# Kernel optimization log

Hardware: AMD Instinct MI355X
Metric: run time of the kernel (lower is better)

Reference implementation:

```python
import jax, jax.numpy as jnp
import numpy as np

B, T, C = 2, 2048, 1024
H, D = 16, 64


def setup_inputs() -> dict:
    key = jax.random.key(0)
    ks = jax.random.split(key, 5)
    s = 1.0 / np.sqrt(C)  # keep projections well-scaled
    return {
        "x": jax.random.normal(ks[0], (B, T, C), dtype=jnp.float32),
        "wq": jax.random.normal(ks[1], (C, C), dtype=jnp.float32) * s,
        "wk": jax.random.normal(ks[2], (C, C), dtype=jnp.float32) * s,
        "wv": jax.random.normal(ks[3], (C, C), dtype=jnp.float32) * s,
        "wo": jax.random.normal(ks[4], (C, C), dtype=jnp.float32) * s,
    }


def reference(x, wq, wk, wv, wo):
    # nn.Linear(d,d,bias=False): y = x @ W.T ; weights stored [out,in]
    q = (x @ wq.T).reshape(B, T, H, D).transpose(0, 2, 1, 3)  # [B,H,T,D]
    k = (x @ wk.T).reshape(B, T, H, D).transpose(0, 2, 1, 3)
    v = (x @ wv.T).reshape(B, T, H, D).transpose(0, 2, 1, 3)
    scale = jnp.sqrt(jnp.float32(D))
    scores = jnp.einsum("bhtd,bhsd->bhts", q, k) / scale  # [B,H,T,T]
    # additive causal mask: -inf above the diagonal
    causal = jnp.tril(jnp.ones((T, T), dtype=bool))
    scores = jnp.where(causal[None, None], scores, jnp.float32(-1e9))
    weights = jax.nn.softmax(scores, axis=-1)
    out = jnp.einsum("bhts,bhsd->bhtd", weights, v)  # [B,H,T,D]
    out = out.transpose(0, 2, 1, 3).reshape(B, T, C)
    return out @ wo.T
```

## Files before the change

### kernel.cpp

```cpp
#include <hip/hip_runtime.h>
#include <stdint.h>

#define B_ 2
#define T_ 2048
#define C_ 1024
#define H_ 16
#define D_ 64
#define M_ (B_*T_)

typedef __attribute__((ext_vector_type(8))) short bf16x8;
typedef __attribute__((ext_vector_type(4))) short bf16x4;
typedef __attribute__((ext_vector_type(4))) float f32x4;
typedef unsigned short u16;

#define MFMA32(a, b, c) __builtin_amdgcn_mfma_f32_16x16x32_bf16((a), (b), (c), 0, 0, 0)

__device__ __forceinline__ u16 f2bf(float f) {
  union { float f; uint32_t u; } v; v.f = f;
  uint32_t u = v.u;
  return (u16)((u + 0x7fffu + ((u >> 16) & 1u)) >> 16);
}

__device__ __forceinline__ float exp2_fast(float x) { return __builtin_amdgcn_exp2f(x); }

typedef const __attribute__((address_space(1))) void* gas_t;
typedef __attribute__((address_space(3))) void* las_t;
__device__ __forceinline__ void gld_lds16(const void* g, void* l) {
  __builtin_amdgcn_global_load_lds((gas_t)g, (las_t)l, 16, 0, 0);
}

__global__ void cvt_bf16(const float* __restrict__ src, u16* __restrict__ dst) {
  int i = (blockIdx.x * blockDim.x + threadIdx.x) * 4;
  float4 v = *(const float4*)(src + i);
  ushort4 o;
  o.x = f2bf(v.x); o.y = f2bf(v.y); o.z = f2bf(v.z); o.w = f2bf(v.w);
  *(ushort4*)(dst + i) = o;
}

__global__ void cvt_bf16_w4(const float* __restrict__ s0, const float* __restrict__ s1,
                            const float* __restrict__ s2, const float* __restrict__ s3,
                            u16* __restrict__ d0, u16* __restrict__ d1,
                            u16* __restrict__ d2, u16* __restrict__ d3) {
  const float* s; u16* d;
  switch (blockIdx.y) {
    case 0: s = s0; d = d0; break;
    case 1: s = s1; d = d1; break;
    case 2: s = s2; d = d2; break;
    default: s = s3; d = d3; break;
  }
  int i = (blockIdx.x * blockDim.x + threadIdx.x) * 4;
  float4 v = *(const float4*)(s + i);
  ushort4 o;
  o.x = f2bf(v.x); o.y = f2bf(v.y); o.z = f2bf(v.z); o.w = f2bf(v.w);
  *(ushort4*)(d + i) = o;
}

__device__ __forceinline__ void gemm_core(const u16* __restrict__ A,
                                          const u16* __restrict__ W,
                                          int m0, int n0, int Kt,
                                          f32x4 acc[4][4])
{
  __shared__ u16 As[128*64];
  __shared__ u16 Bs[128*64];
  const int t = threadIdx.x;
  const int lane = t & 63;
  const int wave = t >> 6;
  const int q = lane >> 4;
  const int l15 = lane & 15;
  const int wm = (wave >> 1) * 64;
  const int wn = (wave & 1) * 64;

  #pragma unroll
  for (int i = 0; i < 4; ++i)
    #pragma unroll
    for (int j = 0; j < 4; ++j)
      acc[i][j] = (f32x4){0.f, 0.f, 0.f, 0.f};

  for (int k0 = 0; k0 < Kt; k0 += 64) {
    #pragma unroll
    for (int r = 0; r < 4; ++r) {
      int Lc = r * 256 + t;
      int row = Lc >> 3;
      int gcc = (Lc & 7) ^ (row & 7);
      gld_lds16(A + (size_t)(m0 + row) * Kt + k0 + gcc * 8, As + Lc * 8);
    }
    #pragma unroll
    for (int r = 0; r < 4; ++r) {
      int Lc = r * 256 + t;
      int row = Lc >> 3;
      int gcc = (Lc & 7) ^ (row & 7);
      gld_lds16(W + (size_t)(n0 + row) * Kt + k0 + gcc * 8, Bs + Lc * 8);
    }
    __syncthreads();

    #pragma unroll
    for (int kk = 0; kk < 2; ++kk) {
      bf16x8 af[4], bfr[4];
      #pragma unroll
      for (int i = 0; i < 4; ++i) {
        int m = wm + i * 16 + l15;
        int ch = (kk * 4 + q) ^ (m & 7);
        af[i] = *(const bf16x8*)(As + m * 64 + ch * 8);
      }
      #pragma unroll
      for (int j = 0; j < 4; ++j) {
        int n = wn + j * 16 + l15;
        int ch = (kk * 4 + q) ^ (n & 7);
        bfr[j] = *(const bf16x8*)(Bs + n * 64 + ch * 8);
      }
      #pragma unroll
      for (int i = 0; i < 4; ++i)
        #pragma unroll
        for (int j = 0; j < 4; ++j)
          acc[i][j] = MFMA32(af[i], bfr[j], acc[i][j]);
    }
    __syncthreads();
  }
}

#define QSCALE 0.1803368801111244f
__global__ __launch_bounds__(256, 3)
void gemm_qkv(const u16* __restrict__ X,
              const u16* __restrict__ Wq, const u16* __restrict__ Wk,
              const u16* __restrict__ Wv,
              u16* __restrict__ Q, u16* __restrict__ K, u16* __restrict__ Vt)
{
  const int bm = blockIdx.x;
  const int bn = blockIdx.y;
  const int seg = bn >> 3;
  const int n0 = (bn & 7) * 128;
  const u16* W = (seg == 0) ? Wq : ((seg == 1) ? Wk : Wv);

  f32x4 acc[4][4];
  gemm_core(X, W, bm * 128, n0, C_, acc);

  const int t = threadIdx.x, lane = t & 63, wave = t >> 6;
  const int q = lane >> 4, l15 = lane & 15;
  const int wm = (wave >> 1) * 64, wn = (wave & 1) * 64;
  const float scale = (seg == 0) ? QSCALE : 1.0f;

  #pragma unroll
  for (int i = 0; i < 4; ++i) {
    #pragma unroll
    for (int j = 0; j < 4; ++j) {
      const int mbase = bm * 128 + wm + i * 16 + q * 4;
      const int n = n0 + wn + j * 16 + l15;
      const int h = n >> 6, d = n & 63;
      if (seg < 2) {
        u16* dst = (seg == 0) ? Q : K;
        #pragma unroll
        for (int r = 0; r < 4; ++r) {
          const int m = mbase + r;
          const int b = m >> 11, tt = m & (T_ - 1);
          size_t idx = (((size_t)(b * H_ + h)) * T_ + tt) * D_ + d;
          dst[idx] = f2bf(acc[i][j][r] * scale);
        }
      } else {
        const int b = mbase >> 11, tt = mbase & (T_ - 1);
        const int ttp = (tt & ~31) | ((tt & 12) << 1) | ((tt & 16) >> 2);
        size_t idx = (((size_t)(b * H_ + h)) * D_ + d) * T_ + ttp;
        ushort4 pk;
        pk.x = f2bf(acc[i][j][0]); pk.y = f2bf(acc[i][j][1]);
        pk.z = f2bf(acc[i][j][2]); pk.w = f2bf(acc[i][j][3]);
        *(ushort4*)(Vt + idx) = pk;
      }
    }
  }
}

__global__ __launch_bounds__(256, 2)
void attn(const u16* __restrict__ Q, const u16* __restrict__ K,
          const u16* __restrict__ Vt, u16* __restrict__ Att)
{
  __shared__ u16 Ks[2][64 * 64];
  __shared__ u16 Vs[2][64 * 64];
  const int t = threadIdx.x;
  const int lane = t & 63, wave = t >> 6;
  const int q = lane >> 4, l15 = lane & 15;
  const int pr = blockIdx.x;
  const int bh = blockIdx.y;
  const int qbA = pr * 64;
  const int qbB = (31 - pr) * 64;
  const u16* Qp = Q + (size_t)bh * T_ * D_;
  const u16* Kp = K + (size_t)bh * T_ * D_;
  const u16* Vp = Vt + (size_t)bh * D_ * T_;

  const int rowA = qbA + 4 * l15 + wave;
  const int rowB = qbB + 4 * l15 + wave;
  const u16* qra = Qp + (size_t)rowA * 64;
  const u16* qrb = Qp + (size_t)rowB * 64;
  const bf16x8 aqA0 = *(const bf16x8*)(qra + q * 8);
  const bf16x8 aqA1 = *(const bf16x8*)(qra + 32 + q * 8);
  const bf16x8 aqB0 = *(const bf16x8*)(qrb + q * 8);
  const bf16x8 aqB1 = *(const bf16x8*)(qrb + 32 + q * 8);

  f32x4 oA[4], oB[4];
  #pragma unroll
  for (int j = 0; j < 4; ++j) {
    oA[j] = (f32x4){0.f, 0.f, 0.f, 0.f};
    oB[j] = (f32x4){0.f, 0.f, 0.f, 0.f};
  }
  float lsA = 0.f, lsB = 0.f;

  auto stage = [&](int kb, int buf) {
    #pragma unroll
    for (int r = 0; r < 2; ++r) {
      int c = r * 256 + t, row = c >> 3, gcc = (c & 7) ^ (row & 7);
      gld_lds16(Kp + (size_t)(kb + row) * 64 + gcc * 8, &Ks[buf][c * 8]);
    }
    #pragma unroll
    for (int r = 0; r < 2; ++r) {
      int c = r * 256 + t, row = c >> 3, gcc = (c & 7) ^ (row & 7);
      gld_lds16(Vp + (size_t)row * T_ + kb + gcc * 8, &Vs[buf][c * 8]);
    }
  };

  stage(0, 0);
  int cur = 0;
  for (int kb = 0; kb <= qbB; kb += 64, cur ^= 1) {
    __syncthreads();
    if (kb + 64 <= qbB) stage(kb + 64, cur ^ 1);
    const u16* Kc = &Ks[cur][0];
    const u16* Vc = &Vs[cur][0];

    bf16x8 kf0[4], kf1[4];
    #pragma unroll
    for (int j2 = 0; j2 < 4; ++j2) {
      const int row = j2 * 16 + l15;
      kf0[j2] = *(const bf16x8*)(Kc + row * 64 + ((q)     ^ (row & 7)) * 8);
      kf1[j2] = *(const bf16x8*)(Kc + row * 64 + ((4 + q) ^ (row & 7)) * 8);
    }
    bf16x8 vfrag[4][2];
    #pragma unroll
    for (int j = 0; j < 4; ++j) {
      const int row = j * 16 + l15;
      #pragma unroll
      for (int kk = 0; kk < 2; ++kk) {
        const int ch = (kk * 4 + q) ^ (row & 7);
        vfrag[j][kk] = *(const bf16x8*)(Vc + row * 64 + ch * 8);
      }
    }

    auto tile_compute = [&](const bf16x8 a0, const bf16x8 a1, f32x4* o,
                            float& lsum, int rowg, bool diag) {
      bf16x4 pb[4];
      #pragma unroll
      for (int j2 = 0; j2 < 4; ++j2) {
        f32x4 z = (f32x4){0.f, 0.f, 0.f, 0.f};
        z = MFMA32(kf0[j2], a0, z);
        z = MFMA32(kf1[j2], a1, z);
        if (diag) {
          #pragma unroll
          for (int r = 0; r < 4; ++r) {
            const int key = kb + j2 * 16 + q * 4 + r;
            if (key > rowg) z[r] = -1e30f;
          }
        }
        float p0 = exp2_fast(z[0]), p1 = exp2_fast(z[1]);
        float p2 = exp2_fast(z[2]), p3 = exp2_fast(z[3]);
        lsum += (p0 + p1) + (p2 + p3);
        pb[j2] = (bf16x4){(short)f2bf(p0), (short)f2bf(p1),
                          (short)f2bf(p2), (short)f2bf(p3)};
      }
      #pragma unroll
      for (int kk = 0; kk < 2; ++kk) {
        const bf16x8 pc = __builtin_shufflevector(pb[2 * kk], pb[2 * kk + 1],
                                                  0, 1, 2, 3, 4, 5, 6, 7);
        #pragma unroll
        for (int j = 0; j < 4; ++j)
          o[j] = MFMA32(vfrag[j][kk], pc, o[j]);
      }
    };

    tile_compute(aqB0, aqB1, oB, lsB, rowB, kb == qbB);
    if (kb <= qbA)
      tile_compute(aqA0, aqA1, oA, lsA, rowA, kb == qbA);
  }

  lsA += __shfl_xor(lsA, 16, 64); lsA += __shfl_xor(lsA, 32, 64);
  lsB += __shfl_xor(lsB, 16, 64); lsB += __shfl_xor(lsB, 32, 64);
  const float invA = __builtin_amdgcn_rcpf(lsA);
  const float invB = __builtin_amdgcn_rcpf(lsB);

  const int b = bh >> 4, h = bh & 15;
  #pragma unroll
  for (int j = 0; j < 4; ++j) {
    ushort4 pa, pbk;
    pa.x = f2bf(oA[j][0] * invA); pa.y = f2bf(oA[j][1] * invA);
    pa.z = f2bf(oA[j][2] * invA); pa.w = f2bf(oA[j][3] * invA);
    pbk.x = f2bf(oB[j][0] * invB); pbk.y = f2bf(oB[j][1] * invB);
    pbk.z = f2bf(oB[j][2] * invB); pbk.w = f2bf(oB[j][3] * invB);
    *(ushort4*)(Att + ((size_t)b * T_ + rowA) * C_ + h * 64 + j * 16 + q * 4) = pa;
    *(ushort4*)(Att + ((size_t)b * T_ + rowB) * C_ + h * 64 + j * 16 + q * 4) = pbk;
  }
}

__global__ __launch_bounds__(256, 2)
void gemm_out(const u16* __restrict__ Att, const u16* __restrict__ Wo,
              float* __restrict__ Out)
{
  __shared__ u16 As[64 * 64];
  __shared__ u16 Bs[128 * 64];
  const int t = threadIdx.x;
  const int lane = t & 63, wave = t >> 6;
  const int q = lane >> 4, l15 = lane & 15;
  const int wm = (wave >> 1) * 32, wn = (wave & 1) * 64;
  const int m0 = blockIdx.x * 64, n0 = blockIdx.y * 128;

  f32x4 acc[2][4];
  #pragma unroll
  for (int i = 0; i < 2; ++i)
    #pragma unroll
    for (int j = 0; j < 4; ++j)
      acc[i][j] = (f32x4){0.f, 0.f, 0.f, 0.f};

  for (int k0 = 0; k0 < C_; k0 += 64) {
    #pragma unroll
    for (int r = 0; r < 2; ++r) {
      int Lc = r * 256 + t, row = Lc >> 3, gcc = (Lc & 7) ^ (row & 7);
      gld_lds16(Att + (size_t)(m0 + row) * C_ + k0 + gcc * 8, As + Lc * 8);
    }
    #pragma unroll
    for (int r = 0; r < 4; ++r) {
      int Lc = r * 256 + t, row = Lc >> 3, gcc = (Lc & 7) ^ (row & 7);
      gld_lds16(Wo + (size_t)(n0 + row) * C_ + k0 + gcc * 8, Bs + Lc * 8);
    }
    __syncthreads();

    #pragma unroll
    for (int kk = 0; kk < 2; ++kk) {
      bf16x8 af[2], bfr[4];
      #pragma unroll
      for (int i = 0; i < 2; ++i) {
        int m = wm + i * 16 + l15;
        int ch = (kk * 4 + q) ^ (m & 7);
        af[i] = *(const bf16x8*)(As + m * 64 + ch * 8);
      }
      #pragma unroll
      for (int j = 0; j < 4; ++j) {
        int n = wn + j * 16 + l15;
        int ch = (kk * 4 + q) ^ (n & 7);
        bfr[j] = *(const bf16x8*)(Bs + n * 64 + ch * 8);
      }
      #pragma unroll
      for (int i = 0; i < 2; ++i)
        #pragma unroll
        for (int j = 0; j < 4; ++j)
          acc[i][j] = MFMA32(af[i], bfr[j], acc[i][j]);
    }
    __syncthreads();
  }

  #pragma unroll
  for (int i = 0; i < 2; ++i) {
    #pragma unroll
    for (int j = 0; j < 4; ++j) {
      const int mm = m0 + wm + i * 16 + q * 4;
      const int n = n0 + wn + j * 16 + l15;
      #pragma unroll
      for (int r = 0; r < 4; ++r)
        Out[(size_t)(mm + r) * C_ + n] = acc[i][j][r];
    }
  }
}

extern "C" void kernel_launch(void* const* d_in, const int* in_sizes, int n_in,
                              void* d_out, int out_size, void* d_ws, size_t ws_size,
                              hipStream_t stream) {
  const float* x  = (const float*)d_in[0];
  const float* wq = (const float*)d_in[1];
  const float* wk = (const float*)d_in[2];
  const float* wv = (const float*)d_in[3];
  const float* wo = (const float*)d_in[4];
  float* out = (float*)d_out;

  u16* ws  = (u16*)d_ws;
  u16* xb  = ws;
  u16* wqb = xb  + (size_t)M_ * C_;
  u16* wkb = wqb + (size_t)C_ * C_;
  u16* wvb = wkb + (size_t)C_ * C_;
  u16* wob = wvb + (size_t)C_ * C_;
  u16* Qb  = wob + (size_t)C_ * C_;
  u16* Kb  = Qb  + (size_t)M_ * C_;
  u16* Vtb = Kb  + (size_t)M_ * C_;
  u16* Atb = Vtb + (size_t)M_ * C_;

  cvt_bf16<<<dim3(M_ * C_ / 1024), 256, 0, stream>>>(x, xb);
  cvt_bf16_w4<<<dim3(C_ * C_ / 1024, 4), 256, 0, stream>>>(wq, wk, wv, wo,
                                                           wqb, wkb, wvb, wob);

  gemm_qkv<<<dim3(M_ / 128, 24), 256, 0, stream>>>(xb, wqb, wkb, wvb, Qb, Kb, Vtb);
  attn<<<dim3(16, B_ * H_), 256, 0, stream>>>(Qb, Kb, Vtb, Atb);
  gemm_out<<<dim3(M_ / 64, C_ / 128), 256, 0, stream>>>(Atb, wob, out);
}
```

Before: 171.8 us.

## Transpose GEMM operands for vector stores and split attention into per-tile blocks

The Q/K projection and the output projection now compute the transposed product (weights as the M operand, tokens as N), so each lane holds four consecutive output features and can write them with one vector store instead of four scattered scalar stores. The attention kernel drops the paired long/short query-tile scheme and launches one block per query tile, heaviest first, with a higher occupancy target in launch bounds. This removes the strided scalar epilogue writes and shrinks the attention register footprint, at the cost of less balanced per-block work and more blocks that stage K/V separately.

```diff
diff --git a/kernel.cpp b/kernel.cpp
--- a/kernel.cpp
+++ b/kernel.cpp
@@ -128,35 +128,43 @@
   const int bm = blockIdx.x;
   const int bn = blockIdx.y;
   const int seg = bn >> 3;
-  const int n0 = (bn & 7) * 128;
-  const u16* W = (seg == 0) ? Wq : ((seg == 1) ? Wk : Wv);
-
-  f32x4 acc[4][4];
-  gemm_core(X, W, bm * 128, n0, C_, acc);
+  const int nb = (bn & 7) * 128;
 
   const int t = threadIdx.x, lane = t & 63, wave = t >> 6;
   const int q = lane >> 4, l15 = lane & 15;
   const int wm = (wave >> 1) * 64, wn = (wave & 1) * 64;
-  const float scale = (seg == 0) ? QSCALE : 1.0f;
-
-  #pragma unroll
-  for (int i = 0; i < 4; ++i) {
-    #pragma unroll
-    for (int j = 0; j < 4; ++j) {
-      const int mbase = bm * 128 + wm + i * 16 + q * 4;
-      const int n = n0 + wn + j * 16 + l15;
-      const int h = n >> 6, d = n & 63;
-      if (seg < 2) {
-        u16* dst = (seg == 0) ? Q : K;
-        #pragma unroll
-        for (int r = 0; r < 4; ++r) {
-          const int m = mbase + r;
-          const int b = m >> 11, tt = m & (T_ - 1);
-          size_t idx = (((size_t)(b * H_ + h)) * T_ + tt) * D_ + d;
-          dst[idx] = f2bf(acc[i][j][r] * scale);
-        }
-      } else {
+
+  f32x4 acc[4][4];
+
+  if (seg < 2) {
+    const u16* W = (seg == 0) ? Wq : Wk;
+    gemm_core(W, X, nb, bm * 128, C_, acc);
+    u16* dst = (seg == 0) ? Q : K;
+    const float scale = (seg == 0) ? QSCALE : 1.0f;
+    #pragma unroll
+    for (int i = 0; i < 4; ++i) {
+      #pragma unroll
+      for (int j = 0; j < 4; ++j) {
+        const int o = nb + wm + i * 16 + q * 4;
+        const int h = o >> 6, d = o & 63;
+        const int mtok = bm * 128 + wn + j * 16 + l15;
+        const int b = mtok >> 11, tt = mtok & (T_ - 1);
+        ushort4 pk;
+        pk.x = f2bf(acc[i][j][0] * scale); pk.y = f2bf(acc[i][j][1] * scale);
+        pk.z = f2bf(acc[i][j][2] * scale); pk.w = f2bf(acc[i][j][3] * scale);
+        *(ushort4*)(dst + (((size_t)(b * H_ + h)) * T_ + tt) * D_ + d) = pk;
+      }
+    }
+  } else {
+    gemm_core(X, Wv, bm * 128, nb, C_, acc);
+    #pragma unroll
+    for (int i = 0; i < 4; ++i) {
+      #pragma unroll
+      for (int j = 0; j < 4; ++j) {
+        const int mbase = bm * 128 + wm + i * 16 + q * 4;
         const int b = mbase >> 11, tt = mbase & (T_ - 1);
+        const int n = nb + wn + j * 16 + l15;
+        const int h = n >> 6, d = n & 63;
         const int ttp = (tt & ~31) | ((tt & 12) << 1) | ((tt & 16) >> 2);
         size_t idx = (((size_t)(b * H_ + h)) * D_ + d) * T_ + ttp;
         ushort4 pk;
@@ -168,7 +176,7 @@
   }
 }
 
-__global__ __launch_bounds__(256, 2)
+__global__ __launch_bounds__(256, 4)
 void attn(const u16* __restrict__ Q, const u16* __restrict__ K,
           const u16* __restrict__ Vt, u16* __restrict__ Att)
 {
@@ -177,121 +185,102 @@
   const int t = threadIdx.x;
   const int lane = t & 63, wave = t >> 6;
   const int q = lane >> 4, l15 = lane & 15;
-  const int pr = blockIdx.x;
+  const int qi = 31 - (int)blockIdx.x;
   const int bh = blockIdx.y;
-  const int qbA = pr * 64;
-  const int qbB = (31 - pr) * 64;
+  const int qb = qi * 64;
   const u16* Qp = Q + (size_t)bh * T_ * D_;
   const u16* Kp = K + (size_t)bh * T_ * D_;
   const u16* Vp = Vt + (size_t)bh * D_ * T_;
 
-  const int rowA = qbA + 4 * l15 + wave;
-  const int rowB = qbB + 4 * l15 + wave;
-  const u16* qra = Qp + (size_t)rowA * 64;
-  const u16* qrb = Qp + (size_t)rowB * 64;
-  const bf16x8 aqA0 = *(const bf16x8*)(qra + q * 8);
-  const bf16x8 aqA1 = *(const bf16x8*)(qra + 32 + q * 8);
-  const bf16x8 aqB0 = *(const bf16x8*)(qrb + q * 8);
-  const bf16x8 aqB1 = *(const bf16x8*)(qrb + 32 + q * 8);
-
-  f32x4 oA[4], oB[4];
-  #pragma unroll
-  for (int j = 0; j < 4; ++j) {
-    oA[j] = (f32x4){0.f, 0.f, 0.f, 0.f};
-    oB[j] = (f32x4){0.f, 0.f, 0.f, 0.f};
-  }
-  float lsA = 0.f, lsB = 0.f;
+  const int row = qb + 4 * l15 + wave;
+  const u16* qr = Qp + (size_t)row * 64;
+  const bf16x8 aq0 = *(const bf16x8*)(qr + q * 8);
+  const bf16x8 aq1 = *(const bf16x8*)(qr + 32 + q * 8);
+
+  f32x4 o[4];
+  #pragma unroll
+  for (int j = 0; j < 4; ++j) o[j] = (f32x4){0.f, 0.f, 0.f, 0.f};
+  float ls = 0.f;
 
   auto stage = [&](int kb, int buf) {
     #pragma unroll
     for (int r = 0; r < 2; ++r) {
-      int c = r * 256 + t, row = c >> 3, gcc = (c & 7) ^ (row & 7);
-      gld_lds16(Kp + (size_t)(kb + row) * 64 + gcc * 8, &Ks[buf][c * 8]);
+      int c = r * 256 + t, rw = c >> 3, gcc = (c & 7) ^ (rw & 7);
+      gld_lds16(Kp + (size_t)(kb + rw) * 64 + gcc * 8, &Ks[buf][c * 8]);
     }
     #pragma unroll
     for (int r = 0; r < 2; ++r) {
-      int c = r * 256 + t, row = c >> 3, gcc = (c & 7) ^ (row & 7);
-      gld_lds16(Vp + (size_t)row * T_ + kb + gcc * 8, &Vs[buf][c * 8]);
+      int c = r * 256 + t, rw = c >> 3, gcc = (c & 7) ^ (rw & 7);
+      gld_lds16(Vp + (size_t)rw * T_ + kb + gcc * 8, &Vs[buf][c * 8]);
     }
   };
 
   stage(0, 0);
   int cur = 0;
-  for (int kb = 0; kb <= qbB; kb += 64, cur ^= 1) {
-    __syncthreads();
-    if (kb + 64 <= qbB) stage(kb + 64, cur ^ 1);
+  for (int kb = 0; kb <= qb; kb += 64, cur ^= 1) {
+    __syncthreads();
+    if (kb + 64 <= qb) stage(kb + 64, cur ^ 1);
     const u16* Kc = &Ks[cur][0];
     const u16* Vc = &Vs[cur][0];
 
     bf16x8 kf0[4], kf1[4];
     #pragma unroll
     for (int j2 = 0; j2 < 4; ++j2) {
-      const int row = j2 * 16 + l15;
-      kf0[j2] = *(const bf16x8*)(Kc + row * 64 + ((q)     ^ (row & 7)) * 8);
-      kf1[j2] = *(const bf16x8*)(Kc + row * 64 + ((4 + q) ^ (row & 7)) * 8);
+      const int rw = j2 * 16 + l15;
+      kf0[j2] = *(const bf16x8*)(Kc + rw * 64 + ((q)     ^ (rw & 7)) * 8);
+      kf1[j2] = *(const bf16x8*)(Kc + rw * 64 + ((4 + q) ^ (rw & 7)) * 8);
     }
     bf16x8 vfrag[4][2];
     #pragma unroll
     for (int j = 0; j < 4; ++j) {
-      const int row = j * 16 + l15;
+      const int rw = j * 16 + l15;
       #pragma unroll
       for (int kk = 0; kk < 2; ++kk) {
-        const int ch = (kk * 4 + q) ^ (row & 7);
-        vfrag[j][kk] = *(const bf16x8*)(Vc + row * 64 + ch * 8);
-      }
-    }
-
-    auto tile_compute = [&](const bf16x8 a0, const bf16x8 a1, f32x4* o,
-                            float& lsum, int rowg, bool diag) {
-      bf16x4 pb[4];
-      #pragma unroll
-      for (int j2 = 0; j2 < 4; ++j2) {
-        f32x4 z = (f32x4){0.f, 0.f, 0.f, 0.f};
-        z = MFMA32(kf0[j2], a0, z);
-        z = MFMA32(kf1[j2], a1, z);
-        if (diag) {
-          #pragma unroll
-          for (int r = 0; r < 4; ++r) {
-            const int key = kb + j2 * 16 + q * 4 + r;
-            if (key > rowg) z[r] = -1e30f;
-          }
+        const int ch = (kk * 4 + q) ^ (rw & 7);
+        vfrag[j][kk] = *(const bf16x8*)(Vc + rw * 64 + ch * 8);
+      }
+    }
+
+    bf16x4 pb[4];
+    const bool diag = (kb == qb);
+    #pragma unroll
+    for (int j2 = 0; j2 < 4; ++j2) {
+      f32x4 z = (f32x4){0.f, 0.f, 0.f, 0.f};
+      z = MFMA32(kf0[j2], aq0, z);
+      z = MFMA32(kf1[j2], aq1, z);
+      if (diag) {
+        #pragma unroll
+        for (int r = 0; r < 4; ++r) {
+          const int key = kb + j2 * 16 + q * 4 + r;
+          if (key > row) z[r] = -1e30f;
         }
-        float p0 = exp2_fast(z[0]), p1 = exp2_fast(z[1]);
-        float p2 = exp2_fast(z[2]), p3 = exp2_fast(z[3]);
-        lsum += (p0 + p1) + (p2 + p3);
-        pb[j2] = (bf16x4){(short)f2bf(p0), (short)f2bf(p1),
-                          (short)f2bf(p2), (short)f2bf(p3)};
-      }
-      #pragma unroll
-      for (int kk = 0; kk < 2; ++kk) {
-        const bf16x8 pc = __builtin_shufflevector(pb[2 * kk], pb[2 * kk + 1],
-                                                  0, 1, 2, 3, 4, 5, 6, 7);
-        #pragma unroll
-        for (int j = 0; j < 4; ++j)
-          o[j] = MFMA32(vfrag[j][kk], pc, o[j]);
-      }
-    };
-
-    tile_compute(aqB0, aqB1, oB, lsB, rowB, kb == qbB);
-    if (kb <= qbA)
-      tile_compute(aqA0, aqA1, oA, lsA, rowA, kb == qbA);
-  }
-
-  lsA += __shfl_xor(lsA, 16, 64); lsA += __shfl_xor(lsA, 32, 64);
-  lsB += __shfl_xor(lsB, 16, 64); lsB += __shfl_xor(lsB, 32, 64);
-  const float invA = __builtin_amdgcn_rcpf(lsA);
-  const float invB = __builtin_amdgcn_rcpf(lsB);
+      }
+      float p0 = exp2_fast(z[0]), p1 = exp2_fast(z[1]);
+      float p2 = exp2_fast(z[2]), p3 = exp2_fast(z[3]);
+      ls += (p0 + p1) + (p2 + p3);
+      pb[j2] = (bf16x4){(short)f2bf(p0), (short)f2bf(p1),
+                        (short)f2bf(p2), (short)f2bf(p3)};
+    }
+    #pragma unroll
+    for (int kk = 0; kk < 2; ++kk) {
+      const bf16x8 pc = __builtin_shufflevector(pb[2 * kk], pb[2 * kk + 1],
+                                                0, 1, 2, 3, 4, 5, 6, 7);
+      #pragma unroll
+      for (int j = 0; j < 4; ++j)
+        o[j] = MFMA32(vfrag[j][kk], pc, o[j]);
+    }
+  }
+
+  ls += __shfl_xor(ls, 16, 64); ls += __shfl_xor(ls, 32, 64);
+  const float inv = __builtin_amdgcn_rcpf(ls);
 
   const int b = bh >> 4, h = bh & 15;
   #pragma unroll
   for (int j = 0; j < 4; ++j) {
-    ushort4 pa, pbk;
-    pa.x = f2bf(oA[j][0] * invA); pa.y = f2bf(oA[j][1] * invA);
-    pa.z = f2bf(oA[j][2] * invA); pa.w = f2bf(oA[j][3] * invA);
-    pbk.x = f2bf(oB[j][0] * invB); pbk.y = f2bf(oB[j][1] * invB);
-    pbk.z = f2bf(oB[j][2] * invB); pbk.w = f2bf(oB[j][3] * invB);
-    *(ushort4*)(Att + ((size_t)b * T_ + rowA) * C_ + h * 64 + j * 16 + q * 4) = pa;
-    *(ushort4*)(Att + ((size_t)b * T_ + rowB) * C_ + h * 64 + j * 16 + q * 4) = pbk;
+    ushort4 pa;
+    pa.x = f2bf(o[j][0] * inv); pa.y = f2bf(o[j][1] * inv);
+    pa.z = f2bf(o[j][2] * inv); pa.w = f2bf(o[j][3] * inv);
+    *(ushort4*)(Att + ((size_t)b * T_ + row) * C_ + h * 64 + j * 16 + q * 4) = pa;
   }
 }
 
@@ -305,7 +294,8 @@
   const int lane = t & 63, wave = t >> 6;
   const int q = lane >> 4, l15 = lane & 15;
   const int wm = (wave >> 1) * 32, wn = (wave & 1) * 64;
-  const int m0 = blockIdx.x * 64, n0 = blockIdx.y * 128;
+  const int m0 = blockIdx.x * 64;
+  const int n0 = blockIdx.y * 128;
 
   f32x4 acc[2][4];
   #pragma unroll
@@ -318,12 +308,12 @@
     #pragma unroll
     for (int r = 0; r < 2; ++r) {
       int Lc = r * 256 + t, row = Lc >> 3, gcc = (Lc & 7) ^ (row & 7);
-      gld_lds16(Att + (size_t)(m0 + row) * C_ + k0 + gcc * 8, As + Lc * 8);
+      gld_lds16(Wo + (size_t)(m0 + row) * C_ + k0 + gcc * 8, As + Lc * 8);
     }
     #pragma unroll
     for (int r = 0; r < 4; ++r) {
       int Lc = r * 256 + t, row = Lc >> 3, gcc = (Lc & 7) ^ (row & 7);
-      gld_lds16(Wo + (size_t)(n0 + row) * C_ + k0 + gcc * 8, Bs + Lc * 8);
+      gld_lds16(Att + (size_t)(n0 + row) * C_ + k0 + gcc * 8, Bs + Lc * 8);
     }
     __syncthreads();
 
@@ -355,11 +345,10 @@
   for (int i = 0; i < 2; ++i) {
     #pragma unroll
     for (int j = 0; j < 4; ++j) {
-      const int mm = m0 + wm + i * 16 + q * 4;
-      const int n = n0 + wn + j * 16 + l15;
-      #pragma unroll
-      for (int r = 0; r < 4; ++r)
-        Out[(size_t)(mm + r) * C_ + n] = acc[i][j][r];
+      const int o = m0 + wm + i * 16 + q * 4;
+      const int tok = n0 + wn + j * 16 + l15;
+      float4 st = {acc[i][j][0], acc[i][j][1], acc[i][j][2], acc[i][j][3]};
+      *(float4*)(Out + (size_t)tok * C_ + o) = st;
     }
   }
 }
@@ -390,6 +379,6 @@
                                                            wqb, wkb, wvb, wob);
 
   gemm_qkv<<<dim3(M_ / 128, 24), 256, 0, stream>>>(xb, wqb, wkb, wvb, Qb, Kb, Vtb);
-  attn<<<dim3(16, B_ * H_), 256, 0, stream>>>(Qb, Kb, Vtb, Atb);
-  gemm_out<<<dim3(M_ / 64, C_ / 128), 256, 0, stream>>>(Atb, wob, out);
-}
+  attn<<<dim3(32, B_ * H_), 256, 0, stream>>>(Qb, Kb, Vtb, Atb);
+  gemm_out<<<dim3(C_ / 64, M_ / 128), 256, 0, stream>>>(Atb, wob, out);
+}
```

Result: slower. 182.1 us (+6.0%).
